# Kernel optimization log

Hardware: AMD Instinct MI355X
Metric: run time of the kernel (lower is better)

Reference implementation:

```python
import jax, jax.numpy as jnp
import numpy as np

B, T, C, H = 4, 2048, 1024, 16
HD = C // H  # head_dim = 64


def setup_inputs() -> dict:
    key = jax.random.key(0)
    k1, k2, k3 = jax.random.split(key, 3)
    x = jax.random.normal(k1, (B, T, C), dtype=jnp.float32)
    W_qkv = jax.random.normal(k2, (C, 3 * C), dtype=jnp.float32) * (1.0 / np.sqrt(C))
    W_out = jax.random.normal(k3, (C, C), dtype=jnp.float32) * (1.0 / np.sqrt(C))
    return {"x": x, "W_qkv": W_qkv, "W_out": W_out}


def reference(x, W_qkv, W_out):
    Bx, Tx, Cx = x.shape
    qkv = jnp.einsum('btc,cd->btd', x, W_qkv)  # [B,T,3C]
    q, k, v = jnp.split(qkv, 3, axis=-1)
    # [B,T,C] -> [B,H,T,HD]
    q = q.reshape(Bx, Tx, H, HD).transpose(0, 2, 1, 3)
    k = k.reshape(Bx, Tx, H, HD).transpose(0, 2, 1, 3)
    v = v.reshape(Bx, Tx, H, HD).transpose(0, 2, 1, 3)
    scale = 1.0 / jnp.sqrt(jnp.asarray(HD, dtype=x.dtype))
    attn = jnp.einsum('bhqd,bhkd->bhqk', q, k) * scale  # [B,H,T,T]
    causal = jnp.tril(jnp.ones((Tx, Tx), dtype=bool))
    attn = jnp.where(causal, attn, jnp.asarray(-1e9, dtype=attn.dtype))
    attn = jax.nn.softmax(attn, axis=-1)
    out = jnp.einsum('bhqk,bhkd->bhqd', attn, v)  # [B,H,T,HD]
    out = out.transpose(0, 2, 1, 3).reshape(Bx, Tx, Cx)
    return jnp.einsum('btc,cd->btd', out, W_out)
```

## Files before the change

kernel.cpp:

```cpp
#include <hip/hip_runtime.h>
#include <hip/hip_bf16.h>
#include <cstdint>


typedef __attribute__((ext_vector_type(8))) short bf16x8;
typedef __attribute__((ext_vector_type(4))) float f32x4;
typedef __attribute__((ext_vector_type(4))) uint32_t u32x4;

#define MFMA_BF16(a, b, c) __builtin_amdgcn_mfma_f32_16x16x32_bf16((a), (b), (c), 0, 0, 0)

__device__ __forceinline__ ushort f2bf(float f) {
  union { float f; uint32_t u; } x;
  x.f = f;
  uint32_t u = x.u;
  return (ushort)((u + 0x7FFFu + ((u >> 16) & 1u)) >> 16);
}

__device__ __forceinline__ uint32_t cvt_pk_bf16(float lo, float hi) {
  uint32_t r;
  asm("v_cvt_pk_bf16_f32 %0, %1, %2" : "=v"(r) : "v"(lo), "v"(hi));
  return r;
}

__device__ __forceinline__ void gload16(const ushort* g, ushort* l) {
  __builtin_amdgcn_global_load_lds(
      (const __attribute__((address_space(1))) void*)g,
      (__attribute__((address_space(3))) void*)l, 16, 0, 0);
}

__global__ __launch_bounds__(256) void convert_f32_bf16(
    const float* __restrict__ in, ushort* __restrict__ out, int n4) {
  int i = blockIdx.x * 256 + threadIdx.x;
  if (i < n4) {
    float4 v = ((const float4*)in)[i];
    ushort4 o;
    o.x = f2bf(v.x); o.y = f2bf(v.y); o.z = f2bf(v.z); o.w = f2bf(v.w);
    ((ushort4*)out)[i] = o;
  }
}

__global__ __launch_bounds__(256) void transpose_w(
    const float* __restrict__ W, ushort* __restrict__ Wt, int K, int N) {
  __shared__ float tile[32][33];
  const int n0 = blockIdx.x * 32, k0 = blockIdx.y * 32;
  const int tx = threadIdx.x & 31, ty = threadIdx.x >> 5;
#pragma unroll
  for (int i = 0; i < 4; ++i)
    tile[ty + i * 8][tx] = W[(size_t)(k0 + ty + i * 8) * N + n0 + tx];
  __syncthreads();
#pragma unroll
  for (int i = 0; i < 4; ++i)
    Wt[(size_t)(n0 + ty + i * 8) * K + k0 + tx] = f2bf(tile[tx][ty + i * 8]);
}

template <int MODE>
__global__ __launch_bounds__(256) void gemm_bf16_kernel(
    const ushort* __restrict__ A, const ushort* __restrict__ Bt,
    float* __restrict__ C,
    ushort* __restrict__ qb, ushort* __restrict__ kb, ushort* __restrict__ vb,
    int M, int N, int K) {
  __shared__ ushort As[128 * 32];
  __shared__ ushort Bs[128 * 32];
  const int tid = threadIdx.x;
  const int lane = tid & 63;
  const int w = tid >> 6;
  const int wr = w >> 1, wc = w & 1;
  const int l15 = lane & 15, lhi = lane >> 4;
  const int row0 = blockIdx.x * 128, col0 = blockIdx.y * 128;

  const int ch = w * 2;
  const int lr = lane >> 2;
  const int lc = (lane & 3) << 3;
  const ushort* ga0 = A  + (size_t)(row0 + ch * 16 + lr) * K + lc;
  const ushort* ga1 = A  + (size_t)(row0 + ch * 16 + 16 + lr) * K + lc;
  const ushort* gb0 = Bt + (size_t)(col0 + ch * 16 + lr) * K + lc;
  const ushort* gb1 = Bt + (size_t)(col0 + ch * 16 + 16 + lr) * K + lc;
  ushort* la0 = &As[ch * 512];
  ushort* la1 = &As[(ch + 1) * 512];
  ushort* lb0 = &Bs[ch * 512];
  ushort* lb1 = &Bs[(ch + 1) * 512];

  f32x4 acc[4][4] = {};

  for (int k0 = 0; k0 < K; k0 += 32) {
    gload16(ga0 + k0, la0);
    gload16(ga1 + k0, la1);
    gload16(gb0 + k0, lb0);
    gload16(gb1 + k0, lb1);
    __syncthreads();
    bf16x8 af[4], bfr[4];
#pragma unroll
    for (int m = 0; m < 4; ++m)
      af[m] = *(const bf16x8*)&As[(wr * 64 + m * 16 + l15) * 32 + lhi * 8];
#pragma unroll
    for (int n = 0; n < 4; ++n)
      bfr[n] = *(const bf16x8*)&Bs[(wc * 64 + n * 16 + l15) * 32 + lhi * 8];
    __builtin_amdgcn_s_setprio(1);
#pragma unroll
    for (int m = 0; m < 4; ++m)
#pragma unroll
      for (int n = 0; n < 4; ++n)
        acc[m][n] = MFMA_BF16(af[m], bfr[n], acc[m][n]);
    __builtin_amdgcn_s_setprio(0);
    __syncthreads();
  }

  if (MODE == 1) {
#pragma unroll
    for (int m = 0; m < 4; ++m) {
      const int r0 = row0 + wr * 64 + m * 16 + lhi * 4;
#pragma unroll
      for (int n = 0; n < 4; ++n) {
        const int c = col0 + wc * 64 + n * 16 + l15;
#pragma unroll
        for (int j = 0; j < 4; ++j)
          C[(size_t)(r0 + j) * N + c] = acc[m][n][j];
      }
    }
  } else {
    const float QSCALE = 0.18033688011112042f;
#pragma unroll
    for (int m = 0; m < 4; ++m) {
      const int r0 = row0 + wr * 64 + m * 16 + lhi * 4;
      const int b_ = r0 >> 11;
      const int t0 = r0 & 2047;
#pragma unroll
      for (int n = 0; n < 4; ++n) {
        const int c = col0 + wc * 64 + n * 16 + l15;
        const int seg = c >> 10;
        const int cc = c & 1023;
        const int h = cc >> 6, d = cc & 63;
        const size_t bhi = (size_t)(b_ * 16 + h);
        if (seg == 0) {
#pragma unroll
          for (int j = 0; j < 4; ++j)
            qb[(bhi * 2048 + t0 + j) * 64 + d] = f2bf(acc[m][n][j] * QSCALE);
        } else if (seg == 1) {
#pragma unroll
          for (int j = 0; j < 4; ++j)
            kb[(bhi * 2048 + t0 + j) * 64 + d] = f2bf(acc[m][n][j]);
        } else {
          const int pos = (t0 & ~31) + ((t0 & 12) << 1) + ((t0 >> 4) & 1) * 4;
          ushort4 pk;
          pk.x = f2bf(acc[m][n][0]);
          pk.y = f2bf(acc[m][n][1]);
          pk.z = f2bf(acc[m][n][2]);
          pk.w = f2bf(acc[m][n][3]);
          *(ushort4*)(vb + (bhi * 64 + d) * 2048 + pos) = pk;
        }
      }
    }
  }
}

#define QK_TILE(SV, KT)                                                      \
  {                                                                          \
    const int krow = (KT) * 16 + l15;                                        \
    const int sw = krow & 7;                                                 \
    bf16x8 kf0 = *(const bf16x8*)&Ks[cur][krow * 64 + ((lhi ^ sw) * 8)];     \
    bf16x8 kf1 = *(const bf16x8*)&Ks[cur][krow * 64 + (((4 + lhi) ^ sw) * 8)];\
    f32x4 acc_ = {};                                                         \
    acc_ = MFMA_BF16(kf0, qf0, acc_);                                        \
    acc_ = MFMA_BF16(kf1, qf1, acc_);                                        \
    SV = acc_;                                                               \
  }

#define MASK_TILE(SV, KT)                                                    \
  {                                                                          \
    if (key0 + (KT) * 16 + lhi * 4 + 0 > qrow) SV[0] = -INFINITY;            \
    if (key0 + (KT) * 16 + lhi * 4 + 1 > qrow) SV[1] = -INFINITY;            \
    if (key0 + (KT) * 16 + lhi * 4 + 2 > qrow) SV[2] = -INFINITY;            \
    if (key0 + (KT) * 16 + lhi * 4 + 3 > qrow) SV[3] = -INFINITY;            \
  }

#define SM_TILE(SV, W0, W1)                                                  \
  {                                                                          \
    float p0 = exp2f(SV[0] - m_state);                                       \
    float p1 = exp2f(SV[1] - m_state);                                       \
    float p2 = exp2f(SV[2] - m_state);                                       \
    float p3 = exp2f(SV[3] - m_state);                                       \
    lloc += (p0 + p1) + (p2 + p3);                                           \
    W0 = cvt_pk_bf16(p0, p1);                                                \
    W1 = cvt_pk_bf16(p2, p3);                                                \
  }

#define PV_TILE(ON, N)                                                       \
  {                                                                          \
    const int vrow = (N) * 16 + l15;                                         \
    const int sw = vrow & 7;                                                 \
    bf16x8 vf0 = *(const bf16x8*)&Vs[cur][vrow * 64 + ((lhi ^ sw) * 8)];     \
    bf16x8 vf1 = *(const bf16x8*)&Vs[cur][vrow * 64 + (((4 + lhi) ^ sw) * 8)];\
    ON = MFMA_BF16(pf0, vf0, ON);                                            \
    ON = MFMA_BF16(pf1, vf1, ON);                                            \
  }

__global__ __launch_bounds__(256)
__attribute__((amdgpu_waves_per_eu(4, 4)))
void attn_kernel(
    const ushort* __restrict__ Qb, const ushort* __restrict__ Kb,
    const ushort* __restrict__ Vt, ushort* __restrict__ Ab) {
  const int bid = blockIdx.x;
  const int qt = 31 - (bid >> 6);
  const int bh = bid & 63;
  const int tid = threadIdx.x;
  const int lane = tid & 63;
  const int w = tid >> 6;
  const int l15 = lane & 15, lhi = lane >> 4;
  const int qloc = qt * 64 + w * 16;

  __shared__ ushort Ks[2][64 * 64];
  __shared__ ushort Vs[2][64 * 64];

  const size_t qkbase = (size_t)bh * (2048 * 64);
  const size_t vtb = (size_t)bh * (64 * 2048);

  const int srow = w * 16 + (lane >> 3);
  const int sd0 = lane & 7;
  const int slot = (sd0 ^ (srow & 7)) * 8;

  const ushort* kp0 = Kb + qkbase + (size_t)srow * 64 + sd0 * 8;
  const ushort* kp1 = kp0 + 8 * 64;
  const ushort* vp0 = Vt + vtb + (size_t)srow * 2048 + sd0 * 8;
  const ushort* vp1 = vp0 + 8 * 2048;

  bf16x8 qf0 = *(const bf16x8*)(Qb + qkbase + (size_t)(qloc + l15) * 64 + lhi * 8);
  bf16x8 qf1 = *(const bf16x8*)(Qb + qkbase + (size_t)(qloc + l15) * 64 + 32 + lhi * 8);

  uint4 kr0 = *(const uint4*)kp0;
  uint4 kr1 = *(const uint4*)kp1;
  uint4 vr0 = *(const uint4*)vp0;
  uint4 vr1 = *(const uint4*)vp1;
  *(uint4*)&Ks[0][srow * 64 + slot] = kr0;
  *(uint4*)&Ks[0][(srow + 8) * 64 + slot] = kr1;
  *(uint4*)&Vs[0][srow * 64 + slot] = vr0;
  *(uint4*)&Vs[0][(srow + 8) * 64 + slot] = vr1;
  __syncthreads();

  float m_state = -INFINITY, l_state = 0.f;
  f32x4 o0 = {}, o1 = {}, o2 = {}, o3 = {};
  const int qrow = qloc + l15;
  int cur = 0;

  for (int kbt = 0; kbt <= qt; ++kbt) {
    const int key0 = kbt * 64;
    const bool last = (kbt == qt);

    if (!last) {
      const size_t koff = (size_t)(kbt + 1) * 64 * 64;
      kr0 = *(const uint4*)(kp0 + koff);
      kr1 = *(const uint4*)(kp1 + koff);
      vr0 = *(const uint4*)(vp0 + (kbt + 1) * 64);
      vr1 = *(const uint4*)(vp1 + (kbt + 1) * 64);
    }

    f32x4 s0, s1, s2, s3;
    __builtin_amdgcn_s_setprio(1);
    QK_TILE(s0, 0)
    QK_TILE(s1, 1)
    QK_TILE(s2, 2)
    QK_TILE(s3, 3)
    __builtin_amdgcn_s_setprio(0);

    if (last) {
      MASK_TILE(s0, 0)
      MASK_TILE(s1, 1)
      MASK_TILE(s2, 2)
      MASK_TILE(s3, 3)
    }

    float t0 = fmaxf(fmaxf(s0[0], s0[1]), fmaxf(s0[2], s0[3]));
    float t1 = fmaxf(fmaxf(s1[0], s1[1]), fmaxf(s1[2], s1[3]));
    float t2 = fmaxf(fmaxf(s2[0], s2[1]), fmaxf(s2[2], s2[3]));
    float t3 = fmaxf(fmaxf(s3[0], s3[1]), fmaxf(s3[2], s3[3]));
    float tmax = fmaxf(fmaxf(t0, t1), fmaxf(t2, t3));
    tmax = fmaxf(tmax, __shfl_xor(tmax, 16));
    tmax = fmaxf(tmax, __shfl_xor(tmax, 32));

    if (!__all(tmax <= m_state + 8.0f)) {
      const float mnew = fmaxf(m_state, tmax);
      const float alpha = exp2f(m_state - mnew);
      const float a0 = __shfl(alpha, lhi * 4 + 0);
      const float a1 = __shfl(alpha, lhi * 4 + 1);
      const float a2 = __shfl(alpha, lhi * 4 + 2);
      const float a3 = __shfl(alpha, lhi * 4 + 3);
      o0[0] *= a0; o0[1] *= a1; o0[2] *= a2; o0[3] *= a3;
      o1[0] *= a0; o1[1] *= a1; o1[2] *= a2; o1[3] *= a3;
      o2[0] *= a0; o2[1] *= a1; o2[2] *= a2; o2[3] *= a3;
      o3[0] *= a0; o3[1] *= a1; o3[2] *= a2; o3[3] *= a3;
      l_state *= alpha;
      m_state = mnew;
    }

    float lloc = 0.f;
    uint32_t w0, w1, w2, w3, w4, w5, w6, w7;
    SM_TILE(s0, w0, w1)
    SM_TILE(s1, w2, w3)
    SM_TILE(s2, w4, w5)
    SM_TILE(s3, w6, w7)
    lloc += __shfl_xor(lloc, 16);
    lloc += __shfl_xor(lloc, 32);
    l_state += lloc;

    u32x4 pw0 = {w0, w1, w2, w3};
    u32x4 pw1 = {w4, w5, w6, w7};
    bf16x8 pf0 = __builtin_bit_cast(bf16x8, pw0);
    bf16x8 pf1 = __builtin_bit_cast(bf16x8, pw1);

    __builtin_amdgcn_s_setprio(1);
    PV_TILE(o0, 0)
    PV_TILE(o1, 1)
    PV_TILE(o2, 2)
    PV_TILE(o3, 3)
    __builtin_amdgcn_s_setprio(0);

    if (!last) {
      const int nxt = cur ^ 1;
      *(uint4*)&Ks[nxt][srow * 64 + slot] = kr0;
      *(uint4*)&Ks[nxt][(srow + 8) * 64 + slot] = kr1;
      *(uint4*)&Vs[nxt][srow * 64 + slot] = vr0;
      *(uint4*)&Vs[nxt][(srow + 8) * 64 + slot] = vr1;
      cur = nxt;
      __syncthreads();
    }
  }

  const int b_ = bh >> 4, h_ = bh & 15;
#pragma unroll
  for (int j = 0; j < 4; ++j) {
    const float linv = 1.0f / __shfl(l_state, lhi * 4 + j);
    const int t = qloc + lhi * 4 + j;
    const size_t ro = ((size_t)b_ * 2048 + t) * 1024 + h_ * 64;
    Ab[ro + 0 * 16 + l15] = f2bf(o0[j] * linv);
    Ab[ro + 1 * 16 + l15] = f2bf(o1[j] * linv);
    Ab[ro + 2 * 16 + l15] = f2bf(o2[j] * linv);
    Ab[ro + 3 * 16 + l15] = f2bf(o3[j] * linv);
  }
}

extern "C" void kernel_launch(void* const* d_in, const int* in_sizes, int n_in,
                              void* d_out, int out_size, void* d_ws, size_t ws_size,
                              hipStream_t stream) {
  const float* x = (const float*)d_in[0];
  const float* Wqkv = (const float*)d_in[1];
  const float* Wout = (const float*)d_in[2];
  float* out = (float*)d_out;

  ushort* xb    = (ushort*)d_ws;
  ushort* wqkvT = xb + (size_t)8192 * 1024;
  ushort* woutT = wqkvT + (size_t)3072 * 1024;
  ushort* qb    = woutT + (size_t)1024 * 1024;
  ushort* kbuf  = qb + (size_t)64 * 2048 * 64;
  ushort* vbuf  = kbuf + (size_t)64 * 2048 * 64;
  ushort* ab    = vbuf + (size_t)64 * 2048 * 64;

  convert_f32_bf16<<<8192, 256, 0, stream>>>(x, xb, 8192 * 1024 / 4);
  transpose_w<<<dim3(96, 32), 256, 0, stream>>>(Wqkv, wqkvT, 1024, 3072);
  transpose_w<<<dim3(32, 32), 256, 0, stream>>>(Wout, woutT, 1024, 1024);
  gemm_bf16_kernel<0><<<dim3(64, 24), 256, 0, stream>>>(
      xb, wqkvT, nullptr, qb, kbuf, vbuf, 8192, 3072, 1024);
  attn_kernel<<<2048, 256, 0, stream>>>(qb, kbuf, vbuf, ab);
  gemm_bf16_kernel<1><<<dim3(64, 8), 256, 0, stream>>>(
      ab, woutT, out, nullptr, nullptr, nullptr, 8192, 1024, 1024);
}
```

Before: 195.2 us.

## Double-buffer GEMM LDS tiles with K=64 stages and XOR swizzle

Rewrites the bf16 GEMM main loop to use two LDS buffers of 128x64 tiles. The next stage's global-to-LDS load is issued before computing on the current one, and the number of barriers per K-step is cut. An XOR swizzle on the 16-byte chunk index is meant to avoid LDS bank conflicts on the fragment reads. It also pins occupancy to 2 waves per EU and raises LDS use to 64KB per block, which may lower occupancy. The loop relies on gload16 being asynchronous and only syncs once per iteration, so there is a risk of a WAR hazard on the buffer being overwritten.

```diff
diff --git a/kernel.cpp b/kernel.cpp
--- a/kernel.cpp
+++ b/kernel.cpp
@@ -54,13 +54,15 @@
 }
 
 template <int MODE>
-__global__ __launch_bounds__(256) void gemm_bf16_kernel(
+__global__ __launch_bounds__(256)
+__attribute__((amdgpu_waves_per_eu(2, 2)))
+void gemm_bf16_kernel(
     const ushort* __restrict__ A, const ushort* __restrict__ Bt,
     float* __restrict__ C,
     ushort* __restrict__ qb, ushort* __restrict__ kb, ushort* __restrict__ vb,
     int M, int N, int K) {
-  __shared__ ushort As[128 * 32];
-  __shared__ ushort Bs[128 * 32];
+  __shared__ ushort As[2][128 * 64];
+  __shared__ ushort Bs[2][128 * 64];
   const int tid = threadIdx.x;
   const int lane = tid & 63;
   const int w = tid >> 6;
@@ -68,42 +70,58 @@
   const int l15 = lane & 15, lhi = lane >> 4;
   const int row0 = blockIdx.x * 128, col0 = blockIdx.y * 128;
 
-  const int ch = w * 2;
-  const int lr = lane >> 2;
-  const int lc = (lane & 3) << 3;
-  const ushort* ga0 = A  + (size_t)(row0 + ch * 16 + lr) * K + lc;
-  const ushort* ga1 = A  + (size_t)(row0 + ch * 16 + 16 + lr) * K + lc;
-  const ushort* gb0 = Bt + (size_t)(col0 + ch * 16 + lr) * K + lc;
-  const ushort* gb1 = Bt + (size_t)(col0 + ch * 16 + 16 + lr) * K + lc;
-  ushort* la0 = &As[ch * 512];
-  ushort* la1 = &As[(ch + 1) * 512];
-  ushort* lb0 = &Bs[ch * 512];
-  ushort* lb1 = &Bs[(ch + 1) * 512];
+  const int cr = lane >> 3;
+  const int sl = lane & 7;
+  const int gofs = (sl ^ cr) << 3;
+  const ushort* gA = A  + (size_t)(row0 + w * 32 + cr) * K + gofs;
+  const ushort* gB = Bt + (size_t)(col0 + w * 32 + cr) * K + gofs;
+  const int lbase = (w * 32) * 64;
 
   f32x4 acc[4][4] = {};
 
-  for (int k0 = 0; k0 < K; k0 += 32) {
-    gload16(ga0 + k0, la0);
-    gload16(ga1 + k0, la1);
-    gload16(gb0 + k0, lb0);
-    gload16(gb1 + k0, lb1);
+#define G_STAGE(BUF, K0)                                                     \
+  {                                                                          \
+    _Pragma("unroll")                                                        \
+    for (int i = 0; i < 4; ++i) {                                            \
+      gload16(gA + (size_t)(i * 8) * K + (K0), &As[BUF][lbase + i * 512]);   \
+      gload16(gB + (size_t)(i * 8) * K + (K0), &Bs[BUF][lbase + i * 512]);   \
+    }                                                                        \
+  }
+
+  const int nk = K >> 6;
+  G_STAGE(0, 0)
+  __syncthreads();
+
+  for (int t = 0; t < nk; ++t) {
+    const int cur = t & 1;
+    if (t + 1 < nk) G_STAGE(cur ^ 1, (t + 1) << 6)
+
+#pragma unroll
+    for (int kh = 0; kh < 2; ++kh) {
+      bf16x8 af[4], bfr[4];
+#pragma unroll
+      for (int m = 0; m < 4; ++m) {
+        const int row = wr * 64 + m * 16 + l15;
+        const int s = kh * 4 + lhi;
+        af[m] = *(const bf16x8*)&As[cur][row * 64 + ((s ^ (row & 7)) << 3)];
+      }
+#pragma unroll
+      for (int n = 0; n < 4; ++n) {
+        const int row = wc * 64 + n * 16 + l15;
+        const int s = kh * 4 + lhi;
+        bfr[n] = *(const bf16x8*)&Bs[cur][row * 64 + ((s ^ (row & 7)) << 3)];
+      }
+      __builtin_amdgcn_s_setprio(1);
+#pragma unroll
+      for (int m = 0; m < 4; ++m)
+#pragma unroll
+        for (int n = 0; n < 4; ++n)
+          acc[m][n] = MFMA_BF16(af[m], bfr[n], acc[m][n]);
+      __builtin_amdgcn_s_setprio(0);
+    }
     __syncthreads();
-    bf16x8 af[4], bfr[4];
-#pragma unroll
-    for (int m = 0; m < 4; ++m)
-      af[m] = *(const bf16x8*)&As[(wr * 64 + m * 16 + l15) * 32 + lhi * 8];
-#pragma unroll
-    for (int n = 0; n < 4; ++n)
-      bfr[n] = *(const bf16x8*)&Bs[(wc * 64 + n * 16 + l15) * 32 + lhi * 8];
-    __builtin_amdgcn_s_setprio(1);
-#pragma unroll
-    for (int m = 0; m < 4; ++m)
-#pragma unroll
-      for (int n = 0; n < 4; ++n)
-        acc[m][n] = MFMA_BF16(af[m], bfr[n], acc[m][n]);
-    __builtin_amdgcn_s_setprio(0);
-    __syncthreads();
-  }
+  }
+#undef G_STAGE
 
   if (MODE == 1) {
 #pragma unroll
```

Measured after the change: 173.8 us. 1.12x faster.
